# Kernel optimization log

Hardware: AMD Instinct MI355X
Metric: run time of the kernel (lower is better)

## Reference

```python
import jax, jax.numpy as jnp
import numpy as np

N_NODES = 50000
N_EDGES = 800000
IN_DIM = 64
EDGE_DIM = 32
OUT_DIM = 64


def setup_inputs() -> dict:
    key = jax.random.key(0)
    ks = jax.random.split(key, 7)
    x = jax.random.normal(ks[0], (N_NODES, IN_DIM), dtype=jnp.float32)
    edge_index = jax.random.randint(ks[1], (2, N_EDGES), 0, N_NODES, dtype=jnp.int64)
    edge_attr = jax.random.normal(ks[2], (N_EDGES, EDGE_DIM), dtype=jnp.float32)
    scale_msg = 1.0 / np.sqrt(IN_DIM + EDGE_DIM)
    scale_self = 1.0 / np.sqrt(IN_DIM)
    msg_w = jax.random.normal(ks[3], (IN_DIM + EDGE_DIM, OUT_DIM), dtype=jnp.float32) * scale_msg
    msg_b = jax.random.normal(ks[4], (OUT_DIM,), dtype=jnp.float32) * scale_msg
    self_w = jax.random.normal(ks[5], (IN_DIM, OUT_DIM), dtype=jnp.float32) * scale_self
    self_b = jax.random.normal(ks[6], (OUT_DIM,), dtype=jnp.float32) * scale_self
    return {"x": x, "edge_index": edge_index, "edge_attr": edge_attr,
            "msg_w": msg_w, "msg_b": msg_b, "self_w": self_w, "self_b": self_b}


def reference(x, edge_index, edge_attr, msg_w, msg_b, self_w, self_b):
    src = edge_index[0]
    dst = edge_index[1]
    n = x.shape[0]
    # gather source features, concat edge attrs, message linear: [E, out]
    msg_in = jnp.concatenate([x[src], edge_attr], axis=1)
    messages = msg_in @ msg_w + msg_b
    # scatter-mean over destination nodes
    agg = jax.ops.segment_sum(messages, dst, num_segments=n)
    deg = jax.ops.segment_sum(jnp.ones((dst.shape[0],), dtype=x.dtype), dst, num_segments=n)
    deg = jnp.maximum(deg, 1.0)[:, None]
    agg = agg / deg
    return x @ self_w + self_b + agg
```

## Files before the change

### kernel.cpp

```cpp
#include <hip/hip_runtime.h>


constexpr int N_NODES  = 50000;
constexpr int N_EDGES  = 800000;
constexpr int IN_DIM   = 64;
constexpr int EDGE_DIM = 32;
constexpr int OUT_DIM  = 64;
constexpr int CAP      = 48;
constexpr int OVF_CAP  = 65536;

using vf4 = __attribute__((ext_vector_type(4))) float;
using vi2 = __attribute__((ext_vector_type(2))) int;

__device__ __forceinline__ void place_one(int dst, int e, int src,
                                          int* cnt, int2* buckets,
                                          int4* ovf, int* ovf_cur) {
    const int pos = atomicAdd(&cnt[dst], 1);
    if (pos < CAP) {
        buckets[(size_t)dst * CAP + pos] = make_int2(e, src);
    } else {
        const int o = atomicAdd(ovf_cur, 1);
        if (o < OVF_CAP) ovf[o] = make_int4(dst, e, src, 0);
    }
}

__global__ __launch_bounds__(256) void place_bucket_k(
    const int* __restrict__ ei, int* cnt, int2* __restrict__ buckets,
    int4* __restrict__ ovf, int* ovf_cur)
{
    const int t = blockIdx.x * 256 + threadIdx.x;
    if (t * 4 + 3 < N_EDGES) {
        const int4 d4 = ((const int4*)(ei + N_EDGES))[t];
        const int4 s4 = ((const int4*)ei)[t];
        place_one(d4.x, 4 * t + 0, s4.x, cnt, buckets, ovf, ovf_cur);
        place_one(d4.y, 4 * t + 1, s4.y, cnt, buckets, ovf, ovf_cur);
        place_one(d4.z, 4 * t + 2, s4.z, cnt, buckets, ovf, ovf_cur);
        place_one(d4.w, 4 * t + 3, s4.w, cnt, buckets, ovf, ovf_cur);
    } else {
        for (int e = t * 4; e < min(t * 4 + 4, N_EDGES); ++e)
            place_one(ei[N_EDGES + e], e, ei[e], cnt, buckets, ovf, ovf_cur);
    }
}

__global__ __launch_bounds__(256) void aggregate_bucket_k(
    const float* __restrict__ x, const float* __restrict__ ea,
    const int2* __restrict__ buckets, const int* __restrict__ cnt,
    const int4* __restrict__ ovf, const int* __restrict__ ovf_cur,
    float* __restrict__ sum_x, float* __restrict__ sum_ea)
{
    const int lane   = threadIdx.x & 63;
    const int wave   = (blockIdx.x * blockDim.x + threadIdx.x) >> 6;
    const int nwaves = (gridDim.x * blockDim.x) >> 6;

    const int grpx = lane >> 4, colx = lane & 15;
    const int grpe = lane >> 3, cole = lane & 7;

    for (int n0 = wave * 2; n0 < N_NODES; n0 += nwaves * 2) {
        const int  nA   = __builtin_amdgcn_readfirstlane(n0);
        const bool hasB = (n0 + 1 < N_NODES);
        const int  nB   = nA + 1;

        const int cFA = __builtin_amdgcn_readfirstlane(cnt[nA]);
        const int cFB = hasB ? __builtin_amdgcn_readfirstlane(cnt[nB]) : 0;
        const int cA  = min(cFA, CAP);
        const int cB  = min(cFB, CAP);

        int eA = 0, srcA = 0, eB = 0, srcB = 0;
        if (lane < cA) {
            const vi2 p = __builtin_nontemporal_load(
                (const vi2*)buckets + (size_t)nA * CAP + lane);
            eA = p.x; srcA = p.y;
        }
        if (lane < cB) {
            const vi2 p = __builtin_nontemporal_load(
                (const vi2*)buckets + (size_t)nB * CAP + lane);
            eB = p.x; srcB = p.y;
        }

        vf4 axA = {0,0,0,0}, aeA = {0,0,0,0};
        vf4 axB = {0,0,0,0}, aeB = {0,0,0,0};

        const int mMax = max(cA, cB);
        for (int j = 0; j < mMax; j += 16) {
            const int jx0 = j +  0 + grpx, jx1 = j +  4 + grpx;
            const int jx2 = j +  8 + grpx, jx3 = j + 12 + grpx;
            const int je0 = j +  0 + grpe, je1 = j +  8 + grpe;
            const int sA0 = __shfl(srcA, jx0), sA1 = __shfl(srcA, jx1);
            const int sA2 = __shfl(srcA, jx2), sA3 = __shfl(srcA, jx3);
            const int sB0 = __shfl(srcB, jx0), sB1 = __shfl(srcB, jx1);
            const int sB2 = __shfl(srcB, jx2), sB3 = __shfl(srcB, jx3);
            const int fA0 = __shfl(eA, je0),   fA1 = __shfl(eA, je1);
            const int fB0 = __shfl(eB, je0),   fB1 = __shfl(eB, je1);

            vf4 xA0 = {0,0,0,0}, xA1 = {0,0,0,0}, xA2 = {0,0,0,0}, xA3 = {0,0,0,0};
            vf4 xB0 = {0,0,0,0}, xB1 = {0,0,0,0}, xB2 = {0,0,0,0}, xB3 = {0,0,0,0};
            vf4 eA0v = {0,0,0,0}, eA1v = {0,0,0,0};
            vf4 eB0v = {0,0,0,0}, eB1v = {0,0,0,0};

            if (jx0 < cA) xA0 = ((const vf4*)(x + (size_t)sA0 * IN_DIM))[colx];
            if (jx1 < cA) xA1 = ((const vf4*)(x + (size_t)sA1 * IN_DIM))[colx];
            if (jx2 < cA) xA2 = ((const vf4*)(x + (size_t)sA2 * IN_DIM))[colx];
            if (jx3 < cA) xA3 = ((const vf4*)(x + (size_t)sA3 * IN_DIM))[colx];
            if (jx0 < cB) xB0 = ((const vf4*)(x + (size_t)sB0 * IN_DIM))[colx];
            if (jx1 < cB) xB1 = ((const vf4*)(x + (size_t)sB1 * IN_DIM))[colx];
            if (jx2 < cB) xB2 = ((const vf4*)(x + (size_t)sB2 * IN_DIM))[colx];
            if (jx3 < cB) xB3 = ((const vf4*)(x + (size_t)sB3 * IN_DIM))[colx];
            if (je0 < cA) eA0v = __builtin_nontemporal_load(
                (const vf4*)(ea + (size_t)fA0 * EDGE_DIM) + cole);
            if (je1 < cA) eA1v = __builtin_nontemporal_load(
                (const vf4*)(ea + (size_t)fA1 * EDGE_DIM) + cole);
            if (je0 < cB) eB0v = __builtin_nontemporal_load(
                (const vf4*)(ea + (size_t)fB0 * EDGE_DIM) + cole);
            if (je1 < cB) eB1v = __builtin_nontemporal_load(
                (const vf4*)(ea + (size_t)fB1 * EDGE_DIM) + cole);

            axA += (xA0 + xA1) + (xA2 + xA3);
            axB += (xB0 + xB1) + (xB2 + xB3);
            aeA += eA0v + eA1v;
            aeB += eB0v + eB1v;
        }

        if (cFA > CAP || cFB > CAP) {
            const int novf = min(__builtin_amdgcn_readfirstlane(*ovf_cur), OVF_CAP);
            for (int i = 0; i < novf; ++i) {
                const int4 v = ovf[i];
                const bool mA = (v.x == nA), mB = hasB && (v.x == nB);
                if (mA || mB) {
                    if (grpx == 0) {
                        const vf4 t = ((const vf4*)(x + (size_t)v.z * IN_DIM))[colx];
                        if (mA) axA += t; else axB += t;
                    }
                    if (grpe == 0) {
                        const vf4 t = ((const vf4*)(ea + (size_t)v.y * EDGE_DIM))[cole];
                        if (mA) aeA += t; else aeB += t;
                    }
                }
            }
        }

#pragma unroll
        for (int mask = 16; mask < 64; mask <<= 1) {
            axA.x += __shfl_xor(axA.x, mask); axA.y += __shfl_xor(axA.y, mask);
            axA.z += __shfl_xor(axA.z, mask); axA.w += __shfl_xor(axA.w, mask);
            axB.x += __shfl_xor(axB.x, mask); axB.y += __shfl_xor(axB.y, mask);
            axB.z += __shfl_xor(axB.z, mask); axB.w += __shfl_xor(axB.w, mask);
        }
#pragma unroll
        for (int mask = 8; mask < 64; mask <<= 1) {
            aeA.x += __shfl_xor(aeA.x, mask); aeA.y += __shfl_xor(aeA.y, mask);
            aeA.z += __shfl_xor(aeA.z, mask); aeA.w += __shfl_xor(aeA.w, mask);
            aeB.x += __shfl_xor(aeB.x, mask); aeB.y += __shfl_xor(aeB.y, mask);
            aeB.z += __shfl_xor(aeB.z, mask); aeB.w += __shfl_xor(aeB.w, mask);
        }

        if (lane < 16) ((vf4*)(sum_x + (size_t)nA * IN_DIM))[lane] = axA;
        if (lane < 8)  ((vf4*)(sum_ea + (size_t)nA * EDGE_DIM))[lane] = aeA;
        if (hasB) {
            if (lane < 16) ((vf4*)(sum_x + (size_t)nB * IN_DIM))[lane] = axB;
            if (lane < 8)  ((vf4*)(sum_ea + (size_t)nB * EDGE_DIM))[lane] = aeB;
        }
    }
}

__global__ __launch_bounds__(64) void finalize64_k(
    const float* __restrict__ x, const float* sum_x_in,
    const float* __restrict__ sum_ea, const int* __restrict__ cnt,
    const float* __restrict__ msg_w, const float* __restrict__ msg_b,
    const float* __restrict__ self_w, const float* __restrict__ self_b,
    float* out)
{
    const int c = threadIdx.x;

    float wm[96];
    float wsf[64];
#pragma unroll
    for (int k = 0; k < 96; ++k) wm[k] = msg_w[k * OUT_DIM + c];
#pragma unroll
    for (int k = 0; k < 64; ++k) wsf[k] = self_w[k * OUT_DIM + c];
    const float mb = msg_b[c];
    const float sb = self_b[c];

    for (int n0 = blockIdx.x; n0 < N_NODES; n0 += gridDim.x) {
        const int n = __builtin_amdgcn_readfirstlane(n0);

        const float4* r1 = (const float4*)(sum_x_in + (size_t)n * IN_DIM);
        const float4* r2 = (const float4*)(sum_ea   + (size_t)n * EDGE_DIM);
        const float4* r3 = (const float4*)(x        + (size_t)n * IN_DIM);
        const int d = cnt[n];

        float am0 = 0.f, am1 = 0.f, am2 = 0.f, am3 = 0.f;
        float as0 = 0.f, as1 = 0.f, as2 = 0.f, as3 = 0.f;
#pragma unroll
        for (int q = 0; q < 16; ++q) {
            const float4 v = r1[q];
            am0 = fmaf(v.x, wm[4 * q + 0], am0);
            am1 = fmaf(v.y, wm[4 * q + 1], am1);
            am2 = fmaf(v.z, wm[4 * q + 2], am2);
            am3 = fmaf(v.w, wm[4 * q + 3], am3);
        }
#pragma unroll
        for (int q = 0; q < 8; ++q) {
            const float4 v = r2[q];
            am0 = fmaf(v.x, wm[64 + 4 * q + 0], am0);
            am1 = fmaf(v.y, wm[64 + 4 * q + 1], am1);
            am2 = fmaf(v.z, wm[64 + 4 * q + 2], am2);
            am3 = fmaf(v.w, wm[64 + 4 * q + 3], am3);
        }
#pragma unroll
        for (int q = 0; q < 16; ++q) {
            const float4 v = r3[q];
            as0 = fmaf(v.x, wsf[4 * q + 0], as0);
            as1 = fmaf(v.y, wsf[4 * q + 1], as1);
            as2 = fmaf(v.z, wsf[4 * q + 2], as2);
            as3 = fmaf(v.w, wsf[4 * q + 3], as3);
        }

        const float inv  = 1.0f / (float)max(d, 1);
        const float bsel = (d > 0) ? 1.0f : 0.0f;
        const float am   = (am0 + am1) + (am2 + am3);
        const float as   = (as0 + as1) + (as2 + as3);

        out[(size_t)n * OUT_DIM + c] = as + sb + am * inv + mb * bsel;
    }
}

__global__ __launch_bounds__(768) void scatter_fb_k(
    const float* __restrict__ x, const int* __restrict__ ei,
    const float* __restrict__ ea, float* sum_x, float* sum_ea, int* deg)
{
    const int t  = threadIdx.x;
    const int el = t / 96;
    const int k  = t - el * 96;
    const int e  = blockIdx.x * 8 + el;
    if (e >= N_EDGES) return;
    const int dst = ei[N_EDGES + e];
    if (k < IN_DIM) {
        const int src = ei[e];
        atomicAdd(&sum_x[dst * IN_DIM + k], x[src * IN_DIM + k]);
        if (k == 0) atomicAdd(&deg[dst], 1);
    } else {
        const int kk = k - IN_DIM;
        atomicAdd(&sum_ea[dst * EDGE_DIM + kk], ea[e * EDGE_DIM + kk]);
    }
}

extern "C" void kernel_launch(void* const* d_in, const int* in_sizes, int n_in,
                              void* d_out, int out_size, void* d_ws, size_t ws_size,
                              hipStream_t stream) {
    const float* x      = (const float*)d_in[0];
    const int*   ei     = (const int*)d_in[1];
    const float* ea     = (const float*)d_in[2];
    const float* msg_w  = (const float*)d_in[3];
    const float* msg_b  = (const float*)d_in[4];
    const float* self_w = (const float*)d_in[5];
    const float* self_b = (const float*)d_in[6];

    float* out = (float*)d_out;

    int*   cnt     = (int*)d_ws;
    int*   ovf_cur = cnt + N_NODES;
    int2*  buckets = (int2*)(cnt + N_NODES + 16);
    int4*  ovf     = (int4*)(buckets + (size_t)N_NODES * CAP);
    float* sum_ea  = (float*)(ovf + OVF_CAP);
    const size_t need_bucket =
        ((size_t)N_NODES + 16 + 2 * (size_t)N_NODES * CAP + 4 * (size_t)OVF_CAP +
         (size_t)N_NODES * EDGE_DIM) * sizeof(int);

    if (ws_size >= need_bucket) {
        hipMemsetAsync(cnt, 0, (N_NODES + 16) * sizeof(int), stream);
        place_bucket_k<<<(N_EDGES / 4 + 255) / 256, 256, 0, stream>>>(
            ei, cnt, buckets, ovf, ovf_cur);
        aggregate_bucket_k<<<(N_NODES / 2 + 3) / 4, 256, 0, stream>>>(
            x, ea, buckets, cnt, ovf, ovf_cur, out, sum_ea);
        finalize64_k<<<4096, 64, 0, stream>>>(
            x, out, sum_ea, cnt, msg_w, msg_b, self_w, self_b, out);
    } else {
        float* fb_sum_ea = (float*)d_ws;
        int*   deg       = (int*)(fb_sum_ea + (size_t)N_NODES * EDGE_DIM);
        hipMemsetAsync(d_out, 0, (size_t)N_NODES * OUT_DIM * sizeof(float), stream);
        hipMemsetAsync(d_ws, 0, (size_t)N_NODES * (EDGE_DIM + 1) * sizeof(float), stream);
        scatter_fb_k<<<(N_EDGES + 7) / 8, 768, 0, stream>>>(
            x, ei, ea, out, fb_sum_ea, deg);
        finalize64_k<<<4096, 64, 0, stream>>>(
            x, out, fb_sum_ea, deg, msg_w, msg_b, self_w, self_b, out);
    }
}
```

Before: 280.3 us.

## Replace scalar finalize with split-bf16 MFMA GEMM over concatenated features

The final per-node dense transform is rewritten as a 16x16x32 bf16 MFMA GEMM over a concatenated [mean_x, mean_ea, x] row of width 160. Each operand is split into high and low bf16 halves and multiplied three times to approximate fp32 accuracy. The aggregate kernel now divides by degree and writes the split bf16 rows directly. The x conversion into the same buffer runs as extra blocks of the bucket-placement kernel, overlapping it with the edge atomics. This removes the scalar FMA-bound finalize at the cost of extra conversion work and triple MFMA passes, with some precision risk.

```diff
diff --git a/kernel.cpp b/kernel.cpp
--- a/kernel.cpp
+++ b/kernel.cpp
@@ -6,11 +6,26 @@
 constexpr int IN_DIM   = 64;
 constexpr int EDGE_DIM = 32;
 constexpr int OUT_DIM  = 64;
+constexpr int K_CAT    = 160;
 constexpr int CAP      = 48;
 constexpr int OVF_CAP  = 65536;
 
-using vf4 = __attribute__((ext_vector_type(4))) float;
-using vi2 = __attribute__((ext_vector_type(2))) int;
+using vf4   = __attribute__((ext_vector_type(4))) float;
+using vi2   = __attribute__((ext_vector_type(2))) int;
+using vu4   = __attribute__((ext_vector_type(4))) unsigned short;
+using bf8   = __attribute__((ext_vector_type(8))) short;
+using f32x4 = __attribute__((ext_vector_type(4))) float;
+
+__device__ __forceinline__ unsigned short f2bf(float f) {
+    unsigned int u = __float_as_uint(f);
+    return (unsigned short)((u + 0x7fffu + ((u >> 16) & 1u)) >> 16);
+}
+__device__ __forceinline__ float bf2f(unsigned short h) {
+    return __uint_as_float(((unsigned int)h) << 16);
+}
+
+constexpr int PLACE_BLOCKS  = (N_EDGES / 4 + 255) / 256;
+constexpr int XSPLIT_BLOCKS = 200;
 
 __device__ __forceinline__ void place_one(int dst, int e, int src,
                                           int* cnt, int2* buckets,
@@ -24,21 +39,41 @@
     }
 }
 
-__global__ __launch_bounds__(256) void place_bucket_k(
+__global__ __launch_bounds__(256) void place_xsplit_k(
     const int* __restrict__ ei, int* cnt, int2* __restrict__ buckets,
-    int4* __restrict__ ovf, int* ovf_cur)
+    int4* __restrict__ ovf, int* ovf_cur,
+    const float* __restrict__ x, unsigned short* __restrict__ ch,
+    unsigned short* __restrict__ cl)
 {
-    const int t = blockIdx.x * 256 + threadIdx.x;
-    if (t * 4 + 3 < N_EDGES) {
-        const int4 d4 = ((const int4*)(ei + N_EDGES))[t];
-        const int4 s4 = ((const int4*)ei)[t];
-        place_one(d4.x, 4 * t + 0, s4.x, cnt, buckets, ovf, ovf_cur);
-        place_one(d4.y, 4 * t + 1, s4.y, cnt, buckets, ovf, ovf_cur);
-        place_one(d4.z, 4 * t + 2, s4.z, cnt, buckets, ovf, ovf_cur);
-        place_one(d4.w, 4 * t + 3, s4.w, cnt, buckets, ovf, ovf_cur);
+    if (blockIdx.x < PLACE_BLOCKS) {
+        const int t = blockIdx.x * 256 + threadIdx.x;
+        if (t * 4 + 3 < N_EDGES) {
+            const int4 d4 = ((const int4*)(ei + N_EDGES))[t];
+            const int4 s4 = ((const int4*)ei)[t];
+            place_one(d4.x, 4 * t + 0, s4.x, cnt, buckets, ovf, ovf_cur);
+            place_one(d4.y, 4 * t + 1, s4.y, cnt, buckets, ovf, ovf_cur);
+            place_one(d4.z, 4 * t + 2, s4.z, cnt, buckets, ovf, ovf_cur);
+            place_one(d4.w, 4 * t + 3, s4.w, cnt, buckets, ovf, ovf_cur);
+        } else {
+            for (int e = t * 4; e < min(t * 4 + 4, N_EDGES); ++e)
+                place_one(ei[N_EDGES + e], e, ei[e], cnt, buckets, ovf, ovf_cur);
+        }
     } else {
-        for (int e = t * 4; e < min(t * 4 + 4, N_EDGES); ++e)
-            place_one(ei[N_EDGES + e], e, ei[e], cnt, buckets, ovf, ovf_cur);
+        const int base   = (blockIdx.x - PLACE_BLOCKS) * 256 + threadIdx.x;
+        const int stride = XSPLIT_BLOCKS * 256;
+        for (int i = base; i < N_NODES * 16; i += stride) {
+            const vf4 v = ((const vf4*)x)[i];
+            const int n = i >> 4, q = i & 15;
+            vu4 h, l;
+#pragma unroll
+            for (int j = 0; j < 4; ++j) {
+                h[j] = f2bf(v[j]);
+                l[j] = f2bf(v[j] - bf2f(h[j]));
+            }
+            const size_t o = (size_t)n * K_CAT + 96 + 4 * q;
+            *(vu4*)(ch + o) = h;
+            *(vu4*)(cl + o) = l;
+        }
     }
 }
 
@@ -46,7 +81,7 @@
     const float* __restrict__ x, const float* __restrict__ ea,
     const int2* __restrict__ buckets, const int* __restrict__ cnt,
     const int4* __restrict__ ovf, const int* __restrict__ ovf_cur,
-    float* __restrict__ sum_x, float* __restrict__ sum_ea)
+    unsigned short* __restrict__ ch, unsigned short* __restrict__ cl)
 {
     const int lane   = threadIdx.x & 63;
     const int wave   = (blockIdx.x * blockDim.x + threadIdx.x) >> 6;
@@ -153,74 +188,140 @@
             aeB.z += __shfl_xor(aeB.z, mask); aeB.w += __shfl_xor(aeB.w, mask);
         }
 
-        if (lane < 16) ((vf4*)(sum_x + (size_t)nA * IN_DIM))[lane] = axA;
-        if (lane < 8)  ((vf4*)(sum_ea + (size_t)nA * EDGE_DIM))[lane] = aeA;
+        const float invA = 1.0f / (float)max(cFA, 1);
+        const float invB = 1.0f / (float)max(cFB, 1);
+        {
+            unsigned short* rhA = ch + (size_t)nA * K_CAT;
+            unsigned short* rlA = cl + (size_t)nA * K_CAT;
+            if (lane < 16) {
+                vu4 h, l;
+#pragma unroll
+                for (int j = 0; j < 4; ++j) {
+                    const float v = axA[j] * invA;
+                    h[j] = f2bf(v); l[j] = f2bf(v - bf2f(h[j]));
+                }
+                *(vu4*)(rhA + 4 * lane) = h;
+                *(vu4*)(rlA + 4 * lane) = l;
+            }
+            if (lane < 8) {
+                vu4 h, l;
+#pragma unroll
+                for (int j = 0; j < 4; ++j) {
+                    const float v = aeA[j] * invA;
+                    h[j] = f2bf(v); l[j] = f2bf(v - bf2f(h[j]));
+                }
+                *(vu4*)(rhA + 64 + 4 * lane) = h;
+                *(vu4*)(rlA + 64 + 4 * lane) = l;
+            }
+        }
         if (hasB) {
-            if (lane < 16) ((vf4*)(sum_x + (size_t)nB * IN_DIM))[lane] = axB;
-            if (lane < 8)  ((vf4*)(sum_ea + (size_t)nB * EDGE_DIM))[lane] = aeB;
-        }
-    }
-}
-
-__global__ __launch_bounds__(64) void finalize64_k(
-    const float* __restrict__ x, const float* sum_x_in,
-    const float* __restrict__ sum_ea, const int* __restrict__ cnt,
+            unsigned short* rhB = ch + (size_t)nB * K_CAT;
+            unsigned short* rlB = cl + (size_t)nB * K_CAT;
+            if (lane < 16) {
+                vu4 h, l;
+#pragma unroll
+                for (int j = 0; j < 4; ++j) {
+                    const float v = axB[j] * invB;
+                    h[j] = f2bf(v); l[j] = f2bf(v - bf2f(h[j]));
+                }
+                *(vu4*)(rhB + 4 * lane) = h;
+                *(vu4*)(rlB + 4 * lane) = l;
+            }
+            if (lane < 8) {
+                vu4 h, l;
+#pragma unroll
+                for (int j = 0; j < 4; ++j) {
+                    const float v = aeB[j] * invB;
+                    h[j] = f2bf(v); l[j] = f2bf(v - bf2f(h[j]));
+                }
+                *(vu4*)(rhB + 64 + 4 * lane) = h;
+                *(vu4*)(rlB + 64 + 4 * lane) = l;
+            }
+        }
+    }
+}
+
+__global__ __launch_bounds__(256) void finalize_mfma_k(
+    const unsigned short* __restrict__ ch, const unsigned short* __restrict__ cl,
+    const int* __restrict__ cnt,
     const float* __restrict__ msg_w, const float* __restrict__ msg_b,
     const float* __restrict__ self_w, const float* __restrict__ self_b,
-    float* out)
+    float* __restrict__ out)
 {
-    const int c = threadIdx.x;
-
-    float wm[96];
-    float wsf[64];
-#pragma unroll
-    for (int k = 0; k < 96; ++k) wm[k] = msg_w[k * OUT_DIM + c];
-#pragma unroll
-    for (int k = 0; k < 64; ++k) wsf[k] = self_w[k * OUT_DIM + c];
-    const float mb = msg_b[c];
-    const float sb = self_b[c];
-
-    for (int n0 = blockIdx.x; n0 < N_NODES; n0 += gridDim.x) {
-        const int n = __builtin_amdgcn_readfirstlane(n0);
-
-        const float4* r1 = (const float4*)(sum_x_in + (size_t)n * IN_DIM);
-        const float4* r2 = (const float4*)(sum_ea   + (size_t)n * EDGE_DIM);
-        const float4* r3 = (const float4*)(x        + (size_t)n * IN_DIM);
-        const int d = cnt[n];
-
-        float am0 = 0.f, am1 = 0.f, am2 = 0.f, am3 = 0.f;
-        float as0 = 0.f, as1 = 0.f, as2 = 0.f, as3 = 0.f;
-#pragma unroll
-        for (int q = 0; q < 16; ++q) {
-            const float4 v = r1[q];
-            am0 = fmaf(v.x, wm[4 * q + 0], am0);
-            am1 = fmaf(v.y, wm[4 * q + 1], am1);
-            am2 = fmaf(v.z, wm[4 * q + 2], am2);
-            am3 = fmaf(v.w, wm[4 * q + 3], am3);
-        }
-#pragma unroll
-        for (int q = 0; q < 8; ++q) {
-            const float4 v = r2[q];
-            am0 = fmaf(v.x, wm[64 + 4 * q + 0], am0);
-            am1 = fmaf(v.y, wm[64 + 4 * q + 1], am1);
-            am2 = fmaf(v.z, wm[64 + 4 * q + 2], am2);
-            am3 = fmaf(v.w, wm[64 + 4 * q + 3], am3);
-        }
-#pragma unroll
-        for (int q = 0; q < 16; ++q) {
-            const float4 v = r3[q];
-            as0 = fmaf(v.x, wsf[4 * q + 0], as0);
-            as1 = fmaf(v.y, wsf[4 * q + 1], as1);
-            as2 = fmaf(v.z, wsf[4 * q + 2], as2);
-            as3 = fmaf(v.w, wsf[4 * q + 3], as3);
-        }
-
-        const float inv  = 1.0f / (float)max(d, 1);
-        const float bsel = (d > 0) ? 1.0f : 0.0f;
-        const float am   = (am0 + am1) + (am2 + am3);
-        const float as   = (as0 + as1) + (as2 + as3);
-
-        out[(size_t)n * OUT_DIM + c] = as + sb + am * inv + mb * bsel;
+    __shared__ short wfh[1280 * 8];
+    __shared__ short wfl[1280 * 8];
+
+    const int tid  = threadIdx.x;
+    const int lane = tid & 63;
+
+    for (int idx = tid; idx < 1280; idx += 256) {
+        const int ct = idx / 320, rem = idx % 320;
+        const int kt = rem / 64,  l   = rem % 64;
+        const int c  = ct * 16 + (l & 15);
+        const int k0 = kt * 32 + ((l >> 4) << 3);
+#pragma unroll
+        for (int j = 0; j < 8; ++j) {
+            const int k = k0 + j;
+            const float w = (k < 96) ? msg_w[k * OUT_DIM + c]
+                                     : self_w[(k - 96) * OUT_DIM + c];
+            const unsigned short h = f2bf(w);
+            wfh[idx * 8 + j] = (short)h;
+            wfl[idx * 8 + j] = (short)f2bf(w - bf2f(h));
+        }
+    }
+    __syncthreads();
+
+    float mbv[4], sbv[4];
+#pragma unroll
+    for (int ct = 0; ct < 4; ++ct) {
+        mbv[ct] = msg_b[ct * 16 + (lane & 15)];
+        sbv[ct] = self_b[ct * 16 + (lane & 15)];
+    }
+
+    const int wid = blockIdx.x * 4 + (tid >> 6);
+    const int nw  = gridDim.x * 4;
+
+    for (int t = wid; t < N_NODES / 16; t += nw) {
+        const int n0 = t * 16;
+        const size_t abase = (size_t)(n0 + (lane & 15)) * K_CAT + ((lane >> 4) << 3);
+        bf8 ah[5], al[5];
+#pragma unroll
+        for (int kt = 0; kt < 5; ++kt) {
+            ah[kt] = *(const bf8*)(ch + abase + kt * 32);
+            al[kt] = *(const bf8*)(cl + abase + kt * 32);
+        }
+        int dr[4];
+#pragma unroll
+        for (int r = 0; r < 4; ++r)
+            dr[r] = cnt[n0 + ((lane >> 4) << 2) + r];
+
+        f32x4 acc[4] = {{0,0,0,0},{0,0,0,0},{0,0,0,0},{0,0,0,0}};
+#pragma unroll
+        for (int kt = 0; kt < 5; ++kt) {
+#pragma unroll
+            for (int ct = 0; ct < 4; ++ct) {
+                const int e = ((ct * 5 + kt) * 64 + lane) * 8;
+                const bf8 bh = *(const bf8*)(wfh + e);
+                const bf8 bl = *(const bf8*)(wfl + e);
+                acc[ct] = __builtin_amdgcn_mfma_f32_16x16x32_bf16(
+                    ah[kt], bh, acc[ct], 0, 0, 0);
+                acc[ct] = __builtin_amdgcn_mfma_f32_16x16x32_bf16(
+                    al[kt], bh, acc[ct], 0, 0, 0);
+                acc[ct] = __builtin_amdgcn_mfma_f32_16x16x32_bf16(
+                    ah[kt], bl, acc[ct], 0, 0, 0);
+            }
+        }
+
+#pragma unroll
+        for (int ct = 0; ct < 4; ++ct) {
+#pragma unroll
+            for (int r = 0; r < 4; ++r) {
+                const float bsel = (dr[r] > 0) ? 1.0f : 0.0f;
+                const int   row  = n0 + ((lane >> 4) << 2) + r;
+                out[(size_t)row * OUT_DIM + ct * 16 + (lane & 15)] =
+                    acc[ct][r] + mbv[ct] * bsel + sbv[ct];
+            }
+        }
     }
 }
 
@@ -244,6 +345,62 @@
     }
 }
 
+__global__ __launch_bounds__(64) void finalize64_k(
+    const float* __restrict__ x, const float* sum_x_in,
+    const float* __restrict__ sum_ea, const int* __restrict__ cnt,
+    const float* __restrict__ msg_w, const float* __restrict__ msg_b,
+    const float* __restrict__ self_w, const float* __restrict__ self_b,
+    float* out)
+{
+    const int c = threadIdx.x;
+    float wm[96], wsf[64];
+#pragma unroll
+    for (int k = 0; k < 96; ++k) wm[k] = msg_w[k * OUT_DIM + c];
+#pragma unroll
+    for (int k = 0; k < 64; ++k) wsf[k] = self_w[k * OUT_DIM + c];
+    const float mb = msg_b[c];
+    const float sb = self_b[c];
+
+    for (int n0 = blockIdx.x; n0 < N_NODES; n0 += gridDim.x) {
+        const int n = __builtin_amdgcn_readfirstlane(n0);
+        const float4* r1 = (const float4*)(sum_x_in + (size_t)n * IN_DIM);
+        const float4* r2 = (const float4*)(sum_ea   + (size_t)n * EDGE_DIM);
+        const float4* r3 = (const float4*)(x        + (size_t)n * IN_DIM);
+        const int d = cnt[n];
+        float am0 = 0.f, am1 = 0.f, am2 = 0.f, am3 = 0.f;
+        float as0 = 0.f, as1 = 0.f, as2 = 0.f, as3 = 0.f;
+#pragma unroll
+        for (int q = 0; q < 16; ++q) {
+            const float4 v = r1[q];
+            am0 = fmaf(v.x, wm[4 * q + 0], am0);
+            am1 = fmaf(v.y, wm[4 * q + 1], am1);
+            am2 = fmaf(v.z, wm[4 * q + 2], am2);
+            am3 = fmaf(v.w, wm[4 * q + 3], am3);
+        }
+#pragma unroll
+        for (int q = 0; q < 8; ++q) {
+            const float4 v = r2[q];
+            am0 = fmaf(v.x, wm[64 + 4 * q + 0], am0);
+            am1 = fmaf(v.y, wm[64 + 4 * q + 1], am1);
+            am2 = fmaf(v.z, wm[64 + 4 * q + 2], am2);
+            am3 = fmaf(v.w, wm[64 + 4 * q + 3], am3);
+        }
+#pragma unroll
+        for (int q = 0; q < 16; ++q) {
+            const float4 v = r3[q];
+            as0 = fmaf(v.x, wsf[4 * q + 0], as0);
+            as1 = fmaf(v.y, wsf[4 * q + 1], as1);
+            as2 = fmaf(v.z, wsf[4 * q + 2], as2);
+            as3 = fmaf(v.w, wsf[4 * q + 3], as3);
+        }
+        const float inv  = 1.0f / (float)max(d, 1);
+        const float bsel = (d > 0) ? 1.0f : 0.0f;
+        out[(size_t)n * OUT_DIM + c] =
+            ((as0 + as1) + (as2 + as3)) + sb +
+            ((am0 + am1) + (am2 + am3)) * inv + mb * bsel;
+    }
+}
+
 extern "C" void kernel_launch(void* const* d_in, const int* in_sizes, int n_in,
                               void* d_out, int out_size, void* d_ws, size_t ws_size,
                               hipStream_t stream) {
@@ -257,31 +414,35 @@
 
     float* out = (float*)d_out;
 
-    int*   cnt     = (int*)d_ws;
-    int*   ovf_cur = cnt + N_NODES;
-    int2*  buckets = (int2*)(cnt + N_NODES + 16);
-    int4*  ovf     = (int4*)(buckets + (size_t)N_NODES * CAP);
-    float* sum_ea  = (float*)(ovf + OVF_CAP);
+    int*            cnt     = (int*)d_ws;
+    int*            ovf_cur = cnt + N_NODES;
+    int2*           buckets = (int2*)(cnt + N_NODES + 16);
+    int4*           ovf     = (int4*)(buckets + (size_t)N_NODES * CAP);
+    unsigned short* ch      = (unsigned short*)(ovf + OVF_CAP);
+    unsigned short* cl      = ch + (size_t)N_NODES * K_CAT;
     const size_t need_bucket =
-        ((size_t)N_NODES + 16 + 2 * (size_t)N_NODES * CAP + 4 * (size_t)OVF_CAP +
-         (size_t)N_NODES * EDGE_DIM) * sizeof(int);
+        ((size_t)N_NODES + 16 + 2 * (size_t)N_NODES * CAP + 4 * (size_t)OVF_CAP) *
+            sizeof(int) +
+        2 * (size_t)N_NODES * K_CAT * sizeof(unsigned short);
 
     if (ws_size >= need_bucket) {
         hipMemsetAsync(cnt, 0, (N_NODES + 16) * sizeof(int), stream);
-        place_bucket_k<<<(N_EDGES / 4 + 255) / 256, 256, 0, stream>>>(
-            ei, cnt, buckets, ovf, ovf_cur);
+        place_xsplit_k<<<PLACE_BLOCKS + XSPLIT_BLOCKS, 256, 0, stream>>>(
+            ei, cnt, buckets, ovf, ovf_cur, x, ch, cl);
         aggregate_bucket_k<<<(N_NODES / 2 + 3) / 4, 256, 0, stream>>>(
-            x, ea, buckets, cnt, ovf, ovf_cur, out, sum_ea);
+            x, ea, buckets, cnt, ovf, ovf_cur, ch, cl);
+        finalize_mfma_k<<<(N_NODES / 16 + 3) / 4, 256, 0, stream>>>(
+            ch, cl, cnt, msg_w, msg_b, self_w, self_b, out);
+    } else {
+        float* fb_sum_x  = (float*)d_ws;
+        float* fb_sum_ea = fb_sum_x + (size_t)N_NODES * IN_DIM;
+        int*   deg       = (int*)(fb_sum_ea + (size_t)N_NODES * EDGE_DIM);
+        hipMemsetAsync(d_ws, 0,
+                       (size_t)N_NODES * (IN_DIM + EDGE_DIM + 1) * sizeof(float),
+                       stream);
+        scatter_fb_k<<<(N_EDGES + 7) / 8, 768, 0, stream>>>(
+            x, ei, ea, fb_sum_x, fb_sum_ea, deg);
         finalize64_k<<<4096, 64, 0, stream>>>(
-            x, out, sum_ea, cnt, msg_w, msg_b, self_w, self_b, out);
-    } else {
-        float* fb_sum_ea = (float*)d_ws;
-        int*   deg       = (int*)(fb_sum_ea + (size_t)N_NODES * EDGE_DIM);
-        hipMemsetAsync(d_out, 0, (size_t)N_NODES * OUT_DIM * sizeof(float), stream);
-        hipMemsetAsync(d_ws, 0, (size_t)N_NODES * (EDGE_DIM + 1) * sizeof(float), stream);
-        scatter_fb_k<<<(N_EDGES + 7) / 8, 768, 0, stream>>>(
-            x, ei, ea, out, fb_sum_ea, deg);
-        finalize64_k<<<4096, 64, 0, stream>>>(
-            x, out, fb_sum_ea, deg, msg_w, msg_b, self_w, self_b, out);
-    }
-}
+            x, fb_sum_x, fb_sum_ea, deg, msg_w, msg_b, self_w, self_b, out);
+    }
+}
```

Result: no change. 277.8 us (-0.9%).
